# Optimization experiments

Measured on AMD Instinct MI355X. Metric: run time of the kernel, lower is better.

## Reference

```python
import jax, jax.numpy as jnp
import numpy as np
import math

D = 512          # belief_dim
H = 128          # hidden_dim
R = 64           # relation_dim
M = 8192         # max_beliefs
N = 131072       # candidate pairs
INIT_BIAS = math.log(0.4 / 0.6) * -1.0  # = log(1.5) ~ 0.405465


def _linear_params(key, fan_in, fan_out):
    kw, kb = jax.random.split(key)
    bound = 1.0 / math.sqrt(fan_in)
    W = jax.random.uniform(kw, (fan_in, fan_out), minval=-bound, maxval=bound, dtype=jnp.float32)
    b = jax.random.uniform(kb, (fan_out,), minval=-bound, maxval=bound, dtype=jnp.float32)
    return W, b


def setup_inputs() -> dict:
    key = jax.random.key(0)
    ks = jax.random.split(key, 11)
    beliefs = jax.random.normal(ks[0], (M, D), dtype=jnp.float32)
    src_idx = jax.random.randint(ks[1], (N,), 0, M)
    tgt_idx = jax.random.randint(ks[2], (N,), 0, M)
    # proposal_net: 3D -> H -> H//2 -> 1  (last bias = log(1.5))
    pw1, pb1 = _linear_params(ks[3], 3 * D, H)
    pw2, pb2 = _linear_params(ks[4], H, H // 2)
    pw3, _ = _linear_params(ks[5], H // 2, 1)
    pb3 = jnp.full((1,), INIT_BIAS, dtype=jnp.float32)
    # direction_net: 3D -> H//2 -> 1 (sigmoid)
    dw1, db1 = _linear_params(ks[6], 3 * D, H // 2)
    dw2, db2 = _linear_params(ks[7], H // 2, 1)
    # relation_net: 3D -> H -> R
    rw1, rb1 = _linear_params(ks[8], 3 * D, H)
    rw2, rb2 = _linear_params(ks[9], H, R)
    return {
        "beliefs": beliefs, "src_idx": src_idx, "tgt_idx": tgt_idx,
        "pw1": pw1, "pb1": pb1, "pw2": pw2, "pb2": pb2, "pw3": pw3, "pb3": pb3,
        "dw1": dw1, "db1": db1, "dw2": dw2, "db2": db2,
        "rw1": rw1, "rb1": rb1, "rw2": rw2, "rb2": rb2,
    }


def reference(beliefs, src_idx, tgt_idx,
              pw1, pb1, pw2, pb2, pw3, pb3,
              dw1, db1, dw2, db2,
              rw1, rb1, rw2, rb2):
    src = beliefs[src_idx]                       # [N, D] gather
    tgt = beliefs[tgt_idx]                       # [N, D] gather
    feats = jnp.concatenate([src, tgt, jnp.abs(src - tgt)], axis=-1)  # [N, 3D]

    # proposal head -> edge probability
    h = jax.nn.relu(feats @ pw1 + pb1)
    h = jax.nn.relu(h @ pw2 + pb2)
    probs = jax.nn.sigmoid((h @ pw3 + pb3)[:, 0])                     # [N]

    # direction head -> angle in [0, pi/2]
    d = jax.nn.relu(feats @ dw1 + db1)
    directions = jax.nn.sigmoid((d @ dw2 + db2)[:, 0]) * (jnp.pi / 2)  # [N]

    # relation head -> initial relation vectors
    r = jax.nn.relu(feats @ rw1 + rb1)
    relations = r @ rw2 + rb2                                          # [N, R]

    return probs, directions, relations
```

## Files before the change

### kernel.cpp

```cpp
#include <hip/hip_runtime.h>
#include <hip/hip_bf16.h>


#define DD 512
#define K3 1536
#define ROWS 128
#define LDACT 328
#define BUFS 12288

typedef short bf16x8 __attribute__((ext_vector_type(8)));
typedef float f32x4 __attribute__((ext_vector_type(4)));

__device__ inline float b2f(short s) {
    union { float f; unsigned u; } v;
    v.u = ((unsigned)(unsigned short)s) << 16;
    return v.f;
}
__device__ inline short f2b(float f) {
    union { float fl; unsigned u; } v;
    v.fl = f;
    unsigned x = v.u;
    unsigned r = x + 0x7fffu + ((x >> 16) & 1u);
    return (short)(r >> 16);
}
__device__ inline short babsdiff(short a, short b) {
    union { float f; unsigned u; } v;
    v.f = b2f(a) - b2f(b);
    return (short)((v.u & 0x7fffffffu) >> 16);
}

__device__ __forceinline__ int sidx32(int seg, int rt, int lane) {
    return ((seg * 8 + rt) * 64 + lane) * 8;
}

__device__ __forceinline__ void writeStage(short* buf, int rtw, int lnw, int kcb,
                                           bf16x8 s0, bf16x8 s1,
                                           bf16x8 t0, bf16x8 t1) {
    bf16x8 a0, a1;
#pragma unroll
    for (int j = 0; j < 8; j++) {
        a0[j] = babsdiff(s0[j], t0[j]);
        a1[j] = babsdiff(s1[j], t1[j]);
    }
    int l0 = kcb * 16 + lnw, l1 = l0 + 16;
    *(bf16x8*)&buf[sidx32(0, rtw, l0)] = s0;
    *(bf16x8*)&buf[sidx32(0, rtw, l1)] = s1;
    *(bf16x8*)&buf[sidx32(1, rtw, l0)] = t0;
    *(bf16x8*)&buf[sidx32(1, rtw, l1)] = t1;
    *(bf16x8*)&buf[sidx32(2, rtw, l0)] = a0;
    *(bf16x8*)&buf[sidx32(2, rtw, l1)] = a1;
}

__device__ __forceinline__ void stage_f32(const float* bs, const float* bt,
                                          short* buf, int rtw, int lnw, int kcb) {
#pragma unroll
    for (int c = 0; c < 2; c++) {
        bf16x8 sb, tb, ab;
#pragma unroll
        for (int h = 0; h < 2; h++) {
            float4 s4 = ((const float4*)bs)[c * 2 + h];
            float4 t4 = ((const float4*)bt)[c * 2 + h];
            float ss[4] = {s4.x, s4.y, s4.z, s4.w};
            float tt[4] = {t4.x, t4.y, t4.z, t4.w};
#pragma unroll
            for (int e = 0; e < 4; e++) {
                int j = h * 4 + e;
                sb[j] = f2b(ss[e]);
                tb[j] = f2b(tt[e]);
                ab[j] = f2b(fabsf(ss[e] - tt[e]));
            }
        }
        int l16 = (kcb + c) * 16 + lnw;
        *(bf16x8*)&buf[sidx32(0, rtw, l16)] = sb;
        *(bf16x8*)&buf[sidx32(1, rtw, l16)] = tb;
        *(bf16x8*)&buf[sidx32(2, rtw, l16)] = ab;
    }
}

#define WT_ELEMS (320 * 1536)
#define P2T_OFF WT_ELEMS
#define R2T_OFF (WT_ELEMS + 64 * 128)
#define PREP_TOT (WT_ELEMS + 2 * 64 * 128)
#define BEL_ELEMS (8192 * 512)
#define BEL_OFF PREP_TOT

__global__ void prep_kernel(const float* __restrict__ pw1,
                            const float* __restrict__ dw1,
                            const float* __restrict__ rw1,
                            const float* __restrict__ pw2,
                            const float* __restrict__ rw2,
                            const float* __restrict__ beliefs,
                            short* __restrict__ ws, int total8) {
    int i8 = blockIdx.x * 256 + threadIdx.x;
    if (i8 >= total8) return;
    int i = i8 * 8;
    bf16x8 o;
    if (i < WT_ELEMS) {
        int n = i / K3, k = i - n * K3;
        const float* src;
        int stride, off;
        if (n < 128)      { src = pw1; stride = 128; off = n; }
        else if (n < 192) { src = dw1; stride = 64;  off = n - 128; }
        else              { src = rw1; stride = 128; off = n - 192; }
#pragma unroll
        for (int j = 0; j < 8; j++) o[j] = f2b(src[(k + j) * stride + off]);
    } else if (i < R2T_OFF) {
        int jj = i - P2T_OFF;
        int n = jj >> 7, k = jj & 127;
#pragma unroll
        for (int j = 0; j < 8; j++) o[j] = f2b(pw2[(k + j) * 64 + n]);
    } else if (i < PREP_TOT) {
        int jj = i - R2T_OFF;
        int n = jj >> 7, k = jj & 127;
#pragma unroll
        for (int j = 0; j < 8; j++) o[j] = f2b(rw2[(k + j) * 64 + n]);
    } else {
        const float4* b4 = (const float4*)(beliefs + (i - BEL_OFF));
        float4 x = b4[0], y = b4[1];
        float v[8] = {x.x, x.y, x.z, x.w, y.x, y.y, y.z, y.w};
#pragma unroll
        for (int j = 0; j < 8; j++) o[j] = f2b(v[j]);
    }
    *(bf16x8*)&ws[i] = o;
}

template<bool BF>
__global__ __launch_bounds__(256, 2) void edge_main(
    const float* __restrict__ beliefs, const short* __restrict__ bel16,
    const int* __restrict__ src_idx, const int* __restrict__ tgt_idx,
    const float* __restrict__ pb1, const float* __restrict__ db1,
    const float* __restrict__ rb1,
    const float* __restrict__ pb2, const float* __restrict__ pw3,
    const float* __restrict__ pb3,
    const float* __restrict__ dw2, const float* __restrict__ db2,
    const float* __restrict__ rb2,
    const short* __restrict__ WT, const short* __restrict__ pw2T,
    const short* __restrict__ rw2T,
    float* __restrict__ out, int N)
{
    __shared__ __align__(16) char smem_u[49152];

    short* As2 = (short*)smem_u;
    short (*acts)[LDACT] = (short (*)[LDACT])smem_u;
    int* sIdx = (int*)smem_u;
    int* tIdx = sIdx + ROWS;

    const int t = threadIdx.x;
    const int r0 = blockIdx.x * ROWS;
    const int w = t >> 6, lane = t & 63, q = lane >> 4, ln = lane & 15;

    if (t < ROWS) sIdx[t] = src_idx[r0 + t] * DD;
    else tIdx[t - ROWS] = tgt_idx[r0 + t - ROWS] * DD;
    __syncthreads();

    const int rrow = t >> 1, kh = t & 1;
    const int rtw = rrow >> 4, lnw = rrow & 15;
    const int kcb = kh * 2;
    const int srow = sIdx[rrow], trow = tIdx[rrow];
    __syncthreads();

    f32x4 acc[5][8];
#pragma unroll
    for (int ct = 0; ct < 5; ct++)
#pragma unroll
        for (int rt = 0; rt < 8; rt++) acc[ct][rt] = (f32x4)(0.f);

    bf16x8 bfr0[5];
#pragma unroll
    for (int ct = 0; ct < 5; ct++) {
        int col = w * 80 + ct * 16 + ln;
        bfr0[ct] = *(const bf16x8*)(WT + (size_t)col * K3 + q * 8);
    }
    if constexpr (BF) {
        const bf16x8* pS = (const bf16x8*)(bel16 + srow + kh * 16);
        const bf16x8* pT = (const bf16x8*)(bel16 + trow + kh * 16);
        writeStage(As2, rtw, lnw, kcb, pS[0], pS[1], pT[0], pT[1]);
    } else {
        stage_f32(beliefs + srow + kh * 16, beliefs + trow + kh * 16,
                  As2, rtw, lnw, kcb);
    }
    __syncthreads();

    for (int step = 0; step < 16; ++step) {
        short* bufC = As2 + (step & 1) * BUFS;
        short* bufN = As2 + ((step & 1) ^ 1) * BUFS;
        const int k0 = step * 32;
        const bool pf = (step < 15);
        bf16x8 ns0, ns1, nt0, nt1;

#pragma unroll
        for (int seg = 0; seg < 3; seg++) {
            bf16x8 bfr[5];
            if (seg == 0) {
#pragma unroll
                for (int ct = 0; ct < 5; ct++) bfr[ct] = bfr0[ct];
            } else {
#pragma unroll
                for (int ct = 0; ct < 5; ct++) {
                    int col = w * 80 + ct * 16 + ln;
                    bfr[ct] = *(const bf16x8*)(WT + (size_t)col * K3 +
                                               seg * DD + k0 + q * 8);
                }
            }
            if (seg == 2) {
                __builtin_amdgcn_sched_barrier(0);
                if (pf) {
                    if constexpr (BF) {
                        const bf16x8* pS = (const bf16x8*)(bel16 + srow + k0 + 32 + kh * 16);
                        const bf16x8* pT = (const bf16x8*)(bel16 + trow + k0 + 32 + kh * 16);
                        ns0 = pS[0]; ns1 = pS[1]; nt0 = pT[0]; nt1 = pT[1];
                    }
#pragma unroll
                    for (int ct = 0; ct < 5; ct++) {
                        int col = w * 80 + ct * 16 + ln;
                        bfr0[ct] = *(const bf16x8*)(WT + (size_t)col * K3 +
                                                    k0 + 32 + q * 8);
                    }
                }
                __builtin_amdgcn_sched_barrier(0);
            }
            __builtin_amdgcn_s_setprio(1);
#pragma unroll
            for (int rt = 0; rt < 8; rt++) {
                bf16x8 af = *(const bf16x8*)&bufC[sidx32(seg, rt, lane)];
#pragma unroll
                for (int ct = 0; ct < 5; ct++)
                    acc[ct][rt] = __builtin_amdgcn_mfma_f32_16x16x32_bf16(
                        af, bfr[ct], acc[ct][rt], 0, 0, 0);
            }
            __builtin_amdgcn_s_setprio(0);
        }
        if constexpr (BF) {
            if (pf) writeStage(bufN, rtw, lnw, kcb, ns0, ns1, nt0, nt1);
        } else {
            if (pf) stage_f32(beliefs + srow + k0 + 32 + kh * 16,
                              beliefs + trow + k0 + 32 + kh * 16,
                              bufN, rtw, lnw, kcb);
        }
        __syncthreads();
    }

#pragma unroll
    for (int h = 0; h < 2; h++) {
#pragma unroll
        for (int ct = 0; ct < 5; ct++) {
            int col = w * 80 + ct * 16 + ln;
            float bias = (col < 128) ? pb1[col]
                       : (col < 192) ? db1[col - 128]
                                     : rb1[col - 192];
#pragma unroll
            for (int rt4 = 0; rt4 < 4; rt4++)
#pragma unroll
                for (int i = 0; i < 4; i++) {
                    int lrow = rt4 * 16 + q * 4 + i;
                    float v = acc[ct][h * 4 + rt4][i] + bias;
                    acts[lrow][col] = f2b(fmaxf(v, 0.f));
                }
        }
        __syncthreads();

        {
            f32x4 rc[4];
#pragma unroll
            for (int rt = 0; rt < 4; rt++) rc[rt] = (f32x4)(0.f);
#pragma unroll
            for (int ks = 0; ks < 4; ks++) {
                bf16x8 bfr = *(const bf16x8*)(rw2T + (w * 16 + ln) * 128 +
                                              ks * 32 + q * 8);
#pragma unroll
                for (int rt = 0; rt < 4; rt++) {
                    bf16x8 afr = *(const bf16x8*)&acts[rt * 16 + ln][192 + ks * 32 + q * 8];
                    rc[rt] = __builtin_amdgcn_mfma_f32_16x16x32_bf16(afr, bfr, rc[rt], 0, 0, 0);
                }
            }
            int col = w * 16 + ln;
            float bias = rb2[col];
            float* rel = out + 2 * (size_t)N;
#pragma unroll
            for (int rt = 0; rt < 4; rt++)
#pragma unroll
                for (int i = 0; i < 4; i++) {
                    int grow = r0 + h * 64 + rt * 16 + q * 4 + i;
                    rel[(size_t)grow * 64 + col] = rc[rt][i] + bias;
                }
        }

        f32x4 pc[4];
        {
#pragma unroll
            for (int rt = 0; rt < 4; rt++) pc[rt] = (f32x4)(0.f);
#pragma unroll
            for (int ks = 0; ks < 4; ks++) {
                bf16x8 bfr = *(const bf16x8*)(pw2T + (w * 16 + ln) * 128 +
                                              ks * 32 + q * 8);
#pragma unroll
                for (int rt = 0; rt < 4; rt++) {
                    bf16x8 afr = *(const bf16x8*)&acts[rt * 16 + ln][0 + ks * 32 + q * 8];
                    pc[rt] = __builtin_amdgcn_mfma_f32_16x16x32_bf16(afr, bfr, pc[rt], 0, 0, 0);
                }
            }
        }
        __syncthreads();

        {
            int col = w * 16 + ln;
            float bias = pb2[col];
#pragma unroll
            for (int rt = 0; rt < 4; rt++)
#pragma unroll
                for (int i = 0; i < 4; i++) {
                    int lrow = rt * 16 + q * 4 + i;
                    acts[lrow][col] = f2b(fmaxf(pc[rt][i] + bias, 0.f));
                }
        }
        __syncthreads();

        if (t < 64) {
            float s = pb3[0];
#pragma unroll 8
            for (int k = 0; k < 64; k++) s += b2f(acts[t][k]) * pw3[k];
            float pr = 1.f / (1.f + __expf(-s));
            out[r0 + h * 64 + t] = pr;
        } else if (t < 128) {
            int lrow = t - 64;
            float s = db2[0];
#pragma unroll 8
            for (int k = 0; k < 64; k++) s += b2f(acts[lrow][128 + k]) * dw2[k];
            float dir = (1.f / (1.f + __expf(-s))) * 1.57079632679489662f;
            out[(size_t)N + r0 + h * 64 + lrow] = dir;
        }
        __syncthreads();
    }
}

extern "C" void kernel_launch(void* const* d_in, const int* in_sizes, int n_in,
                              void* d_out, int out_size, void* d_ws, size_t ws_size,
                              hipStream_t stream) {
    const float* beliefs = (const float*)d_in[0];
    const int* src = (const int*)d_in[1];
    const int* tgt = (const int*)d_in[2];
    const float* pw1 = (const float*)d_in[3];
    const float* pb1 = (const float*)d_in[4];
    const float* pw2 = (const float*)d_in[5];
    const float* pb2 = (const float*)d_in[6];
    const float* pw3 = (const float*)d_in[7];
    const float* pb3 = (const float*)d_in[8];
    const float* dw1 = (const float*)d_in[9];
    const float* db1 = (const float*)d_in[10];
    const float* dw2 = (const float*)d_in[11];
    const float* db2 = (const float*)d_in[12];
    const float* rw1 = (const float*)d_in[13];
    const float* rb1 = (const float*)d_in[14];
    const float* rw2 = (const float*)d_in[15];
    const float* rb2 = (const float*)d_in[16];

    short* ws = (short*)d_ws;
    short* WT    = ws;
    short* pw2T  = ws + P2T_OFF;
    short* rw2T  = ws + R2T_OFF;
    short* bel16 = ws + BEL_OFF;
    const int N = in_sizes[1];

    const bool useBf = ws_size >= (size_t)(PREP_TOT + BEL_ELEMS) * sizeof(short);
    const int prepElems = useBf ? (PREP_TOT + BEL_ELEMS) : PREP_TOT;
    const int prep8 = prepElems / 8;

    prep_kernel<<<(prep8 + 255) / 256, 256, 0, stream>>>(
        pw1, dw1, rw1, pw2, rw2, beliefs, ws, prep8);

    if (useBf)
        edge_main<true><<<N / ROWS, 256, 0, stream>>>(
            beliefs, bel16, src, tgt, pb1, db1, rb1, pb2, pw3, pb3,
            dw2, db2, rb2, WT, pw2T, rw2T, (float*)d_out, N);
    else
        edge_main<false><<<N / ROWS, 256, 0, stream>>>(
            beliefs, bel16, src, tgt, pb1, db1, rb1, pb2, pw3, pb3,
            dw2, db2, rb2, WT, pw2T, rw2T, (float*)d_out, N);
}
```

Baseline: 266.4 us.

## Precompute per-belief src/tgt first-layer products and gather them per edge

The first layer is split by linearity. The src and tgt blocks of the fused first-layer weights are applied once per belief (8192 rows) in a new prep_bst kernel that stores fp32 partial results. The main kernel then only runs the |src-tgt| K=512 GEMM per edge, double-buffering the abs-diff staging in LDS, and adds the gathered per-belief partials before the ReLU. This cuts per-edge GEMM work to a third. In exchange it needs a large fp32 workspace, gathers 2x320 floats per edge, and uses more LDS, which may reduce occupancy.

```diff
diff --git a/kernel.cpp b/kernel.cpp
--- a/kernel.cpp
+++ b/kernel.cpp
@@ -7,6 +7,7 @@
 #define ROWS 128
 #define LDACT 328
 #define BUFS 12288
+#define BUFS2 16384
 
 typedef short bf16x8 __attribute__((ext_vector_type(8)));
 typedef float f32x4 __attribute__((ext_vector_type(4)));
@@ -28,20 +29,20 @@
     v.f = b2f(a) - b2f(b);
     return (short)((v.u & 0x7fffffffu) >> 16);
 }
+__device__ __forceinline__ bf16x8 babs8(bf16x8 s, bf16x8 t) {
+    bf16x8 a;
+#pragma unroll
+    for (int j = 0; j < 8; j++) a[j] = babsdiff(s[j], t[j]);
+    return a;
+}
 
 __device__ __forceinline__ int sidx32(int seg, int rt, int lane) {
     return ((seg * 8 + rt) * 64 + lane) * 8;
 }
-
 __device__ __forceinline__ void writeStage(short* buf, int rtw, int lnw, int kcb,
                                            bf16x8 s0, bf16x8 s1,
                                            bf16x8 t0, bf16x8 t1) {
-    bf16x8 a0, a1;
-#pragma unroll
-    for (int j = 0; j < 8; j++) {
-        a0[j] = babsdiff(s0[j], t0[j]);
-        a1[j] = babsdiff(s1[j], t1[j]);
-    }
+    bf16x8 a0 = babs8(s0, t0), a1 = babs8(s1, t1);
     int l0 = kcb * 16 + lnw, l1 = l0 + 16;
     *(bf16x8*)&buf[sidx32(0, rtw, l0)] = s0;
     *(bf16x8*)&buf[sidx32(0, rtw, l1)] = s1;
@@ -50,7 +51,6 @@
     *(bf16x8*)&buf[sidx32(2, rtw, l0)] = a0;
     *(bf16x8*)&buf[sidx32(2, rtw, l1)] = a1;
 }
-
 __device__ __forceinline__ void stage_f32(const float* bs, const float* bt,
                                           short* buf, int rtw, int lnw, int kcb) {
 #pragma unroll
@@ -124,6 +124,254 @@
     *(bf16x8*)&ws[i] = o;
 }
 
+__global__ __launch_bounds__(256) void prep_bst(
+    const short* __restrict__ bel16, const short* __restrict__ WT,
+    float* __restrict__ Bs, float* __restrict__ Bt) {
+    const int tb = blockIdx.x & 1;
+    const int r0 = (blockIdx.x >> 1) * 64;
+    const int t = threadIdx.x;
+    const int w = t >> 6, lane = t & 63, q = lane >> 4, ln = lane & 15;
+    float* Bo = tb ? Bt : Bs;
+    const int koff = tb ? 512 : 0;
+
+    f32x4 acc[5][4];
+#pragma unroll
+    for (int ct = 0; ct < 5; ct++)
+#pragma unroll
+        for (int rt = 0; rt < 4; rt++) acc[ct][rt] = (f32x4)(0.f);
+
+#pragma unroll
+    for (int k0 = 0; k0 < 512; k0 += 128)
+#pragma unroll
+        for (int kk = 0; kk < 4; kk++) {
+            bf16x8 bfr[5];
+#pragma unroll
+            for (int ct = 0; ct < 5; ct++)
+                bfr[ct] = *(const bf16x8*)(WT + (size_t)(w * 80 + ct * 16 + ln) * K3 +
+                                           koff + k0 + kk * 32 + q * 8);
+#pragma unroll
+            for (int rt = 0; rt < 4; rt++) {
+                bf16x8 af = *(const bf16x8*)(bel16 +
+                    (size_t)(r0 + rt * 16 + ln) * DD + k0 + kk * 32 + q * 8);
+#pragma unroll
+                for (int ct = 0; ct < 5; ct++)
+                    acc[ct][rt] = __builtin_amdgcn_mfma_f32_16x16x32_bf16(
+                        af, bfr[ct], acc[ct][rt], 0, 0, 0);
+            }
+        }
+#pragma unroll
+    for (int ct = 0; ct < 5; ct++)
+#pragma unroll
+        for (int rt = 0; rt < 4; rt++)
+#pragma unroll
+            for (int i = 0; i < 4; i++)
+                Bo[(size_t)(r0 + rt * 16 + q * 4 + i) * 320 +
+                   w * 80 + ct * 16 + ln] = acc[ct][rt][i];
+}
+
+__global__ __launch_bounds__(256, 2) void edge_main2(
+    const short* __restrict__ bel16,
+    const int* __restrict__ src_idx, const int* __restrict__ tgt_idx,
+    const float* __restrict__ Bs, const float* __restrict__ Bt,
+    const float* __restrict__ pb1, const float* __restrict__ db1,
+    const float* __restrict__ rb1,
+    const float* __restrict__ pb2, const float* __restrict__ pw3,
+    const float* __restrict__ pb3,
+    const float* __restrict__ dw2, const float* __restrict__ db2,
+    const float* __restrict__ rb2,
+    const short* __restrict__ WT, const short* __restrict__ pw2T,
+    const short* __restrict__ rw2T,
+    float* __restrict__ out, int N)
+{
+    __shared__ __align__(16) char smem_u[65536];
+    __shared__ int sIdxR[ROWS], tIdxR[ROWS];
+    short* As = (short*)smem_u;
+    short (*acts)[LDACT] = (short (*)[LDACT])smem_u;
+
+    const int t = threadIdx.x;
+    const int r0 = blockIdx.x * ROWS;
+    const int w = t >> 6, lane = t & 63, q = lane >> 4, ln = lane & 15;
+
+    if (t < ROWS) sIdxR[t] = src_idx[r0 + t];
+    else tIdxR[t - ROWS] = tgt_idx[r0 + t - ROWS];
+    __syncthreads();
+
+    const int rr = t >> 1, kh = t & 1;
+    const int rtw = rr >> 4, lnw = rr & 15;
+    const size_t srow = (size_t)sIdxR[rr] * DD + kh * 64;
+    const size_t trow = (size_t)tIdxR[rr] * DD + kh * 64;
+
+    f32x4 acc[5][8];
+#pragma unroll
+    for (int ct = 0; ct < 5; ct++)
+#pragma unroll
+        for (int rt = 0; rt < 8; rt++) acc[ct][rt] = (f32x4)(0.f);
+
+#pragma unroll
+    for (int c = 0; c < 8; c++) {
+        bf16x8 s8 = *(const bf16x8*)(bel16 + srow + c * 8);
+        bf16x8 t8 = *(const bf16x8*)(bel16 + trow + c * 8);
+        bf16x8 a8 = babs8(s8, t8);
+        int gg = kh * 8 + c, kd = gg >> 2, qd = gg & 3;
+        *(bf16x8*)&As[((kd * 8 + rtw) * 64 + qd * 16 + lnw) * 8] = a8;
+    }
+    __syncthreads();
+
+#pragma unroll
+    for (int step = 0; step < 4; step++) {
+        short* bufC = As + (step & 1) * BUFS2;
+        short* bufN = As + ((step & 1) ^ 1) * BUFS2;
+        const int k0 = step * 128;
+        const bool pf = (step < 3);
+        bf16x8 ps0, ps1, pt0, pt1;
+
+#pragma unroll
+        for (int kk = 0; kk < 4; kk++) {
+            bf16x8 bfr[5];
+#pragma unroll
+            for (int ct = 0; ct < 5; ct++)
+                bfr[ct] = *(const bf16x8*)(WT + (size_t)(w * 80 + ct * 16 + ln) * K3 +
+                                           1024 + k0 + kk * 32 + q * 8);
+            __builtin_amdgcn_sched_barrier(0);
+            if (pf) {
+                if (kk > 0) {
+                    bf16x8 a0 = babs8(ps0, pt0), a1 = babs8(ps1, pt1);
+                    int g0 = kh * 8 + 2 * (kk - 1);
+                    int kd0 = g0 >> 2, qd0 = g0 & 3;
+                    int g1 = g0 + 1, kd1 = g1 >> 2, qd1 = g1 & 3;
+                    *(bf16x8*)&bufN[((kd0 * 8 + rtw) * 64 + qd0 * 16 + lnw) * 8] = a0;
+                    *(bf16x8*)&bufN[((kd1 * 8 + rtw) * 64 + qd1 * 16 + lnw) * 8] = a1;
+                }
+                ps0 = *(const bf16x8*)(bel16 + srow + k0 + 128 + (2 * kk) * 8);
+                ps1 = *(const bf16x8*)(bel16 + srow + k0 + 128 + (2 * kk + 1) * 8);
+                pt0 = *(const bf16x8*)(bel16 + trow + k0 + 128 + (2 * kk) * 8);
+                pt1 = *(const bf16x8*)(bel16 + trow + k0 + 128 + (2 * kk + 1) * 8);
+            }
+            __builtin_amdgcn_sched_barrier(0);
+            __builtin_amdgcn_s_setprio(1);
+#pragma unroll
+            for (int rt = 0; rt < 8; rt++) {
+                bf16x8 af = *(const bf16x8*)&bufC[((kk * 8 + rt) * 64 + lane) * 8];
+#pragma unroll
+                for (int ct = 0; ct < 5; ct++)
+                    acc[ct][rt] = __builtin_amdgcn_mfma_f32_16x16x32_bf16(
+                        af, bfr[ct], acc[ct][rt], 0, 0, 0);
+            }
+            __builtin_amdgcn_s_setprio(0);
+        }
+        if (pf) {
+            bf16x8 a0 = babs8(ps0, pt0), a1 = babs8(ps1, pt1);
+            int g0 = kh * 8 + 6;
+            int kd0 = g0 >> 2, qd0 = g0 & 3;
+            int g1 = g0 + 1, kd1 = g1 >> 2, qd1 = g1 & 3;
+            *(bf16x8*)&bufN[((kd0 * 8 + rtw) * 64 + qd0 * 16 + lnw) * 8] = a0;
+            *(bf16x8*)&bufN[((kd1 * 8 + rtw) * 64 + qd1 * 16 + lnw) * 8] = a1;
+        }
+        __syncthreads();
+    }
+
+#pragma unroll
+    for (int h = 0; h < 2; h++) {
+        float bias5[5];
+#pragma unroll
+        for (int ct = 0; ct < 5; ct++) {
+            int col = w * 80 + ct * 16 + ln;
+            bias5[ct] = (col < 128) ? pb1[col]
+                      : (col < 192) ? db1[col - 128]
+                                    : rb1[col - 192];
+        }
+#pragma unroll
+        for (int rt4 = 0; rt4 < 4; rt4++)
+#pragma unroll
+            for (int i = 0; i < 4; i++) {
+                int lrow = rt4 * 16 + q * 4 + i;
+                const float* bsp = Bs + (size_t)sIdxR[h * 64 + lrow] * 320 +
+                                   w * 80 + ln;
+                const float* btp = Bt + (size_t)tIdxR[h * 64 + lrow] * 320 +
+                                   w * 80 + ln;
+#pragma unroll
+                for (int ct = 0; ct < 5; ct++) {
+                    float v = acc[ct][h * 4 + rt4][i] +
+                              bsp[ct * 16] + btp[ct * 16] + bias5[ct];
+                    acts[lrow][w * 80 + ct * 16 + ln] = f2b(fmaxf(v, 0.f));
+                }
+            }
+        __syncthreads();
+
+        {
+            f32x4 rc[4];
+#pragma unroll
+            for (int rt = 0; rt < 4; rt++) rc[rt] = (f32x4)(0.f);
+#pragma unroll
+            for (int ks = 0; ks < 4; ks++) {
+                bf16x8 bfr = *(const bf16x8*)(rw2T + (w * 16 + ln) * 128 +
+                                              ks * 32 + q * 8);
+#pragma unroll
+                for (int rt = 0; rt < 4; rt++) {
+                    bf16x8 afr = *(const bf16x8*)&acts[rt * 16 + ln][192 + ks * 32 + q * 8];
+                    rc[rt] = __builtin_amdgcn_mfma_f32_16x16x32_bf16(afr, bfr, rc[rt], 0, 0, 0);
+                }
+            }
+            int col = w * 16 + ln;
+            float bias = rb2[col];
+            float* rel = out + 2 * (size_t)N;
+#pragma unroll
+            for (int rt = 0; rt < 4; rt++)
+#pragma unroll
+                for (int i = 0; i < 4; i++) {
+                    int grow = r0 + h * 64 + rt * 16 + q * 4 + i;
+                    rel[(size_t)grow * 64 + col] = rc[rt][i] + bias;
+                }
+        }
+
+        f32x4 pc[4];
+        {
+#pragma unroll
+            for (int rt = 0; rt < 4; rt++) pc[rt] = (f32x4)(0.f);
+#pragma unroll
+            for (int ks = 0; ks < 4; ks++) {
+                bf16x8 bfr = *(const bf16x8*)(pw2T + (w * 16 + ln) * 128 +
+                                              ks * 32 + q * 8);
+#pragma unroll
+                for (int rt = 0; rt < 4; rt++) {
+                    bf16x8 afr = *(const bf16x8*)&acts[rt * 16 + ln][0 + ks * 32 + q * 8];
+                    pc[rt] = __builtin_amdgcn_mfma_f32_16x16x32_bf16(afr, bfr, pc[rt], 0, 0, 0);
+                }
+            }
+        }
+        __syncthreads();
+
+        {
+            int col = w * 16 + ln;
+            float bias = pb2[col];
+#pragma unroll
+            for (int rt = 0; rt < 4; rt++)
+#pragma unroll
+                for (int i = 0; i < 4; i++) {
+                    int lrow = rt * 16 + q * 4 + i;
+                    acts[lrow][col] = f2b(fmaxf(pc[rt][i] + bias, 0.f));
+                }
+        }
+        __syncthreads();
+
+        if (t < 64) {
+            float s = pb3[0];
+#pragma unroll 8
+            for (int k = 0; k < 64; k++) s += b2f(acts[t][k]) * pw3[k];
+            float pr = 1.f / (1.f + __expf(-s));
+            out[r0 + h * 64 + t] = pr;
+        } else if (t < 128) {
+            int lrow = t - 64;
+            float s = db2[0];
+#pragma unroll 8
+            for (int k = 0; k < 64; k++) s += b2f(acts[lrow][128 + k]) * dw2[k];
+            float dir = (1.f / (1.f + __expf(-s))) * 1.57079632679489662f;
+            out[(size_t)N + r0 + h * 64 + lrow] = dir;
+        }
+        __syncthreads();
+    }
+}
+
 template<bool BF>
 __global__ __launch_bounds__(256, 2) void edge_main(
     const float* __restrict__ beliefs, const short* __restrict__ bel16,
@@ -139,7 +387,6 @@
     float* __restrict__ out, int N)
 {
     __shared__ __align__(16) char smem_u[49152];
-
     short* As2 = (short*)smem_u;
     short (*acts)[LDACT] = (short (*)[LDACT])smem_u;
     int* sIdx = (int*)smem_u;
@@ -258,7 +505,6 @@
                 }
         }
         __syncthreads();
-
         {
             f32x4 rc[4];
 #pragma unroll
@@ -284,7 +530,6 @@
                     rel[(size_t)grow * 64 + col] = rc[rt][i] + bias;
                 }
         }
-
         f32x4 pc[4];
         {
 #pragma unroll
@@ -301,7 +546,6 @@
             }
         }
         __syncthreads();
-
         {
             int col = w * 16 + ln;
             float bias = pb2[col];
@@ -314,7 +558,6 @@
                 }
         }
         __syncthreads();
-
         if (t < 64) {
             float s = pb3[0];
 #pragma unroll 8
@@ -361,19 +604,31 @@
     short* bel16 = ws + BEL_OFF;
     const int N = in_sizes[1];
 
-    const bool useBf = ws_size >= (size_t)(PREP_TOT + BEL_ELEMS) * sizeof(short);
+    const size_t BF_BYTES = (size_t)(PREP_TOT + BEL_ELEMS) * sizeof(short);
+    const size_t FULL_BYTES = BF_BYTES + (size_t)2 * 8192 * 320 * sizeof(float);
+    const bool useV2 = ws_size >= FULL_BYTES;
+    const bool useBf = ws_size >= BF_BYTES;
     const int prepElems = useBf ? (PREP_TOT + BEL_ELEMS) : PREP_TOT;
     const int prep8 = prepElems / 8;
 
     prep_kernel<<<(prep8 + 255) / 256, 256, 0, stream>>>(
         pw1, dw1, rw1, pw2, rw2, beliefs, ws, prep8);
 
-    if (useBf)
+    if (useV2) {
+        float* Bsp = (float*)(ws + PREP_TOT + BEL_ELEMS);
+        float* Btp = Bsp + (size_t)8192 * 320;
+        prep_bst<<<256, 256, 0, stream>>>(bel16, WT, Bsp, Btp);
+        edge_main2<<<N / ROWS, 256, 0, stream>>>(
+            bel16, src, tgt, Bsp, Btp,
+            pb1, db1, rb1, pb2, pw3, pb3, dw2, db2, rb2,
+            WT, pw2T, rw2T, (float*)d_out, N);
+    } else if (useBf) {
         edge_main<true><<<N / ROWS, 256, 0, stream>>>(
             beliefs, bel16, src, tgt, pb1, db1, rb1, pb2, pw3, pb3,
             dw2, db2, rb2, WT, pw2T, rw2T, (float*)d_out, N);
-    else
+    } else {
         edge_main<false><<<N / ROWS, 256, 0, stream>>>(
             beliefs, bel16, src, tgt, pb1, db1, rb1, pb2, pw3, pb3,
             dw2, db2, rb2, WT, pw2T, rw2T, (float*)d_out, N);
-}
+    }
+}
```

New measurement: 251.4 us. 5.6% less time.
